# Kernel optimization log

Hardware: AMD Instinct MI355X
Metric: run time of the kernel (lower is better)

Reference implementation:

```python
import jax, jax.numpy as jnp
import numpy as np

NEG_SLOPE = 0.2  # both GATConv internal LeakyReLU and the module-level activation


def gat_conv(x, src, dst, W, a_src, a_dst, bias):
    """PyG GATConv (concat=True, add_self_loops handled by caller via src/dst).
    x: [N, Din]; W: [Din, H*C]; a_src, a_dst: [H, C]; bias: [H*C]."""
    N = x.shape[0]
    H, C = a_src.shape
    h = (x @ W).reshape(N, H, C)                       # [N, H, C]
    al_src = jnp.einsum('nhc,hc->nh', h, a_src)        # [N, H]
    al_dst = jnp.einsum('nhc,hc->nh', h, a_dst)        # [N, H]
    e = jax.nn.leaky_relu(al_src[src] + al_dst[dst], NEG_SLOPE)  # [E, H]
    # segment softmax over edges grouped by destination node
    m = jax.ops.segment_max(e, dst, num_segments=N)    # [N, H]
    ex = jnp.exp(e - m[dst])
    denom = jax.ops.segment_sum(ex, dst, num_segments=N)
    alpha = ex / denom[dst]                            # [E, H]
    out = jax.ops.segment_sum(alpha[:, :, None] * h[src], dst, num_segments=N)
    return out.reshape(N, H * C) + bias


def setup_inputs() -> dict:
    key = jax.random.key(0)
    N, E = 50000, 800000
    D_IN, HID, H = 128, 128, 2
    C = HID // H
    ks = jax.random.split(key, 20)
    inp = {
        'x': jax.random.normal(ks[0], (N, D_IN), dtype=jnp.float32),
        'edge_index': jax.random.randint(ks[1], (2, E), 0, N, dtype=jnp.int64),
    }
    dims = [D_IN, HID, HID]  # input dims of the 3 GATConv layers
    for i, din in enumerate(dims, start=1):
        s = 1.0 / np.sqrt(din)
        inp[f'W{i}'] = jax.random.normal(ks[2 + 4 * i], (din, HID), dtype=jnp.float32) * s
        inp[f'a_src{i}'] = jax.random.normal(ks[3 + 4 * i], (H, C), dtype=jnp.float32) * 0.1
        inp[f'a_dst{i}'] = jax.random.normal(ks[4 + 4 * i], (H, C), dtype=jnp.float32) * 0.1
        inp[f'b{i}'] = jnp.zeros((HID,), dtype=jnp.float32)
    inp['lin_w'] = jax.random.normal(ks[2], (HID, 1), dtype=jnp.float32) * (1.0 / np.sqrt(HID))
    inp['lin_b'] = jnp.zeros((1,), dtype=jnp.float32)
    return inp


def reference(x, edge_index, W1, a_src1, a_dst1, b1, W2, a_src2, a_dst2, b2,
              W3, a_src3, a_dst3, b3, lin_w, lin_b):
    N = x.shape[0]
    loops = jnp.arange(N, dtype=edge_index.dtype)
    src = jnp.concatenate([edge_index[0], loops])  # add_self_loops=True
    dst = jnp.concatenate([edge_index[1], loops])

    h = jax.nn.leaky_relu(gat_conv(x, src, dst, W1, a_src1, a_dst1, b1), NEG_SLOPE)
    # dropout is identity in eval mode (p=0.0)
    h = jax.nn.leaky_relu(h + gat_conv(h, src, dst, W2, a_src2, a_dst2, b2), NEG_SLOPE)
    h = jax.nn.leaky_relu(h + gat_conv(h, src, dst, W3, a_src3, a_dst3, b3), NEG_SLOPE)
    logits = (h @ lin_w + lin_b).squeeze(-1)  # [N]
    return logits
```

## Files before the change

kernel.cpp:

```cpp
#include <hip/hip_runtime.h>
#include <hip/hip_bf16.h>
#include <hip/hip_fp16.h>

#define LEAK 0.2f
#define BCAP 4096

typedef _Float16 half8  __attribute__((ext_vector_type(8)));
typedef _Float16 half4v __attribute__((ext_vector_type(4)));
typedef float    float4v __attribute__((ext_vector_type(4)));


__global__ __launch_bounds__(256) void k_binscatter(const int* __restrict__ esrc,
                                                    const int* __restrict__ edst,
                                                    int* __restrict__ gcnt,
                                                    unsigned int* __restrict__ binned,
                                                    int E, int ETOT, int NBK, int eb,
                                                    const float* __restrict__ W0,
                                                    const float* __restrict__ W1,
                                                    const float* __restrict__ W2,
                                                    _Float16* __restrict__ w16t) {
    int t = threadIdx.x;
    if (blockIdx.x >= eb) {
        __shared__ _Float16 tile[64][68];
        int bb = blockIdx.x - eb;
        int m = bb >> 2;
        int ti = (bb >> 1) & 1, tj = bb & 1;
        const float* src = (m == 0) ? W0 : (m == 1 ? W1 : W2);
        _Float16* dst = w16t + m * 16384;
        for (int idx = t; idx < 4096; idx += 256) {
            int r = idx >> 6, c = idx & 63;
            tile[r][c] = (_Float16)src[(ti * 64 + r) * 128 + tj * 64 + c];
        }
        __syncthreads();
        for (int idx = t; idx < 4096; idx += 256) {
            int c = idx >> 6, r = idx & 63;
            dst[(tj * 64 + c) * 128 + ti * 64 + r] = tile[r][c];
        }
        return;
    }
    __shared__ int lh[512];
    __shared__ int lbase[512];
    for (int b = t; b < NBK; b += 256) lh[b] = 0;
    __syncthreads();
    int base = blockIdx.x * 4096;
    unsigned int word[16]; int bb[16], rk[16];
    #pragma unroll
    for (int u = 0; u < 16; ++u) {
        int e = base + u * 256 + t;
        bb[u] = -1;
        if (e < ETOT) {
            int s, d;
            if (e < E) { s = esrc[e]; d = edst[e]; } else { s = d = e - E; }
            int b = d >> 7;
            bb[u] = b;
            rk[u] = atomicAdd(&lh[b], 1);
            word[u] = (unsigned int)s | ((unsigned int)(d & 127) << 17);
        }
    }
    __syncthreads();
    for (int b = t; b < NBK; b += 256) {
        int c = lh[b];
        lbase[b] = c ? atomicAdd(&gcnt[b], c) : 0;
    }
    __syncthreads();
    #pragma unroll
    for (int u = 0; u < 16; ++u)
        if (bb[u] >= 0)
            binned[(size_t)bb[u] * BCAP + lbase[bb[u]] + rk[u]] = word[u];
}

__global__ __launch_bounds__(256) void k_scatter2(const unsigned int* __restrict__ binned,
                                                  const int* __restrict__ gcnt,
                                                  int* __restrict__ off,
                                                  int* __restrict__ endv,
                                                  int* __restrict__ csr, int N) {
    __shared__ int deg[128];
    __shared__ int lcur[128];
    __shared__ int wt[2];
    int b = blockIdx.x, t = threadIdx.x;
    int n0 = b << 7;
    if (t < 128) deg[t] = 0;
    __syncthreads();
    int beg = b * BCAP, end = beg + gcnt[b];
    for (int i = beg + t; i < end; i += 256)
        atomicAdd(&deg[binned[i] >> 17], 1);
    __syncthreads();
    int v = 0, x = 0;
    if (t < 128) {
        v = deg[t];
        x = v;
        int lane = t & 63;
        #pragma unroll
        for (int o = 1; o < 64; o <<= 1) {
            int y = __shfl_up(x, o);
            if (lane >= o) x += y;
        }
        if (lane == 63) wt[t >> 6] = x;
    }
    __syncthreads();
    if (t < 128) {
        int excl = x - v + ((t >= 64) ? wt[0] : 0) + beg;
        lcur[t] = excl;
        int node = n0 + t;
        if (node < N) { off[node] = excl; endv[node] = excl + v; }
    }
    __syncthreads();
    for (int i = beg + t; i < end; i += 256) {
        unsigned int u = binned[i];
        int pos = atomicAdd(&lcur[u >> 17], 1);
        csr[pos] = (int)(u & 0x1FFFF);
    }
}


__global__ __launch_bounds__(256) void k_gemm_mfma(const void* __restrict__ Xv, int xfp16,
                                                   const _Float16* __restrict__ WhT,
                                                   const float* __restrict__ a_src,
                                                   const float* __restrict__ a_dst,
                                                   _Float16* __restrict__ Hout,
                                                   float* __restrict__ alsrc,
                                                   float* __restrict__ aldst, int N) {
    __shared__ _Float16 As[64][136];
    __shared__ float sS[64][2];
    __shared__ float sD[64][2];
    const int t = threadIdx.x;
    const int lane = t & 63, w = t >> 6;
    const int block_row = blockIdx.x * 64;

    if (t < 128) { sS[t >> 1][t & 1] = 0.f; sD[t >> 1][t & 1] = 0.f; }

    if (xfp16) {
        const _Float16* Xh = (const _Float16*)Xv;
        #pragma unroll
        for (int it = 0; it < 4; ++it) {
            int i = t + 256 * it;
            int row = i >> 4, c8 = i & 15;
            int gr = block_row + row;
            half8 hv = (half8){0,0,0,0,0,0,0,0};
            if (gr < N) hv = *(const half8*)(Xh + (size_t)gr * 128 + c8 * 8);
            *(half8*)(&As[row][c8 * 8]) = hv;
        }
    } else {
        const float* X = (const float*)Xv;
        #pragma unroll
        for (int it = 0; it < 8; ++it) {
            int i = t + 256 * it;
            int row = i >> 5, c4 = i & 31;
            int gr = block_row + row;
            float4 xv = make_float4(0.f, 0.f, 0.f, 0.f);
            if (gr < N) xv = *(const float4*)(X + (size_t)gr * 128 + c4 * 4);
            half4v hv;
            hv[0] = (_Float16)xv.x; hv[1] = (_Float16)xv.y;
            hv[2] = (_Float16)xv.z; hv[3] = (_Float16)xv.w;
            *(half4v*)(&As[row][c4 * 4]) = hv;
        }
    }

    const int l15 = lane & 15, kq = (lane >> 4) * 8;
    half8 bf[2][4];
    #pragma unroll
    for (int ntl = 0; ntl < 2; ++ntl) {
        int n0 = (w * 2 + ntl) * 16 + l15;
        #pragma unroll
        for (int kt = 0; kt < 4; ++kt)
            bf[ntl][kt] = *(const half8*)(WhT + (size_t)n0 * 128 + kt * 32 + kq);
    }
    __syncthreads();

    float4v acc[4][2];
    #pragma unroll
    for (int mt = 0; mt < 4; ++mt)
        #pragma unroll
        for (int ntl = 0; ntl < 2; ++ntl)
            acc[mt][ntl] = (float4v){0.f, 0.f, 0.f, 0.f};

    #pragma unroll
    for (int kt = 0; kt < 4; ++kt) {
        half8 a[4];
        #pragma unroll
        for (int mt = 0; mt < 4; ++mt)
            a[mt] = *(const half8*)(&As[mt * 16 + l15][kt * 32 + kq]);
        #pragma unroll
        for (int mt = 0; mt < 4; ++mt)
            #pragma unroll
            for (int ntl = 0; ntl < 2; ++ntl)
                acc[mt][ntl] = __builtin_amdgcn_mfma_f32_16x16x32_f16(
                    a[mt], bf[ntl][kt], acc[mt][ntl], 0, 0, 0);
    }

    #pragma unroll
    for (int mt = 0; mt < 4; ++mt) {
        int r0 = block_row + mt * 16 + (lane >> 4) * 4;
        #pragma unroll
        for (int ntl = 0; ntl < 2; ++ntl) {
            int col = (w * 2 + ntl) * 16 + l15;
            #pragma unroll
            for (int reg = 0; reg < 4; ++reg) {
                int r = r0 + reg;
                if (r < N) Hout[(size_t)r * 128 + col] = (_Float16)acc[mt][ntl][reg];
            }
        }
    }

    {
        int c0 = w * 32 + l15, c1 = c0 + 16;
        float as0 = a_src[c0], as1 = a_src[c1];
        float ad0 = a_dst[c0], ad1 = a_dst[c1];
        int head = w >> 1;
        #pragma unroll
        for (int mt = 0; mt < 4; ++mt) {
            #pragma unroll
            for (int reg = 0; reg < 4; ++reg) {
                float ps = (float)acc[mt][0][reg] * as0 + (float)acc[mt][1][reg] * as1;
                float pd = (float)acc[mt][0][reg] * ad0 + (float)acc[mt][1][reg] * ad1;
                #pragma unroll
                for (int o = 1; o < 16; o <<= 1) {
                    ps += __shfl_xor(ps, o);
                    pd += __shfl_xor(pd, o);
                }
                if (l15 == 0) {
                    int row = mt * 16 + (lane >> 4) * 4 + reg;
                    atomicAdd(&sS[row][head], ps);
                    atomicAdd(&sD[row][head], pd);
                }
            }
        }
    }
    __syncthreads();
    if (t < 128) {
        int row = t >> 1, head = t & 1;
        int gr = block_row + row;
        if (gr < N) {
            alsrc[gr * 2 + head] = sS[row][head];
            aldst[gr * 2 + head] = sD[row][head];
        }
    }
}


__global__ __launch_bounds__(256) void k_aggregate(
        const _Float16* __restrict__ H16,
        const float* __restrict__ alsrc,
        const float* __restrict__ aldst,
        const int* __restrict__ off, const int* __restrict__ endv,
        const int* __restrict__ csr,
        const float* __restrict__ bias,
        const _Float16* __restrict__ prev,
        _Float16* __restrict__ Out,
        const float* __restrict__ lw, const float* __restrict__ lb,
        float* __restrict__ logits, int N, int mode) {
    int wglobal = (int)((blockIdx.x * 256 + threadIdx.x) >> 6);
    int lane = threadIdx.x & 63;
    if (wglobal * 2 >= N) return;
    int half = lane >> 5;
    int hl = lane & 31;
    int node = wglobal * 2 + half;
    bool active = node < N;
    int nodeC = active ? node : (N - 1);
    int beg = off[nodeC];
    int end = active ? endv[nodeC] : beg;
    float ad0 = aldst[nodeC * 2], ad1 = aldst[nodeC * 2 + 1];

    int p = hl & 15;
    int q = hl >> 4;
    bool head0 = p < 8;
    const _Float16* hbase = H16 + p * 8;
    int hb = half << 5;

    float acc[8];
    #pragma unroll
    for (int k = 0; k < 8; ++k) acc[k] = 0.f;
    float dsum = 0.f;

    for (int base = beg; base < end; base += 32) {
        int i = base + hl;
        int s = 0; float w0 = 0.f, w1 = 0.f;
        if (i < end) {
            s = csr[i];
            float2 al = *(const float2*)(&alsrc[s * 2]);
            float e0 = al.x + ad0; e0 = e0 > 0.f ? e0 : LEAK * e0;
            float e1 = al.y + ad1; e1 = e1 > 0.f ? e1 : LEAK * e1;
            w0 = __expf(e0); w1 = __expf(e1);
        }
        int cnt = min(32, end - base);
        int iters = (cnt + 1) >> 1;
        int jj = 0;
        for (; jj + 4 <= iters; jj += 4) {
            int sl0 = hb + (jj << 1) + q;
            int sj0 = __shfl(s, sl0), sj1 = __shfl(s, sl0 + 2);
            int sj2 = __shfl(s, sl0 + 4), sj3 = __shfl(s, sl0 + 6);
            float w00 = __shfl(w0, sl0),     w10 = __shfl(w1, sl0);
            float w01 = __shfl(w0, sl0 + 2), w11 = __shfl(w1, sl0 + 2);
            float w02 = __shfl(w0, sl0 + 4), w12 = __shfl(w1, sl0 + 4);
            float w03 = __shfl(w0, sl0 + 6), w13 = __shfl(w1, sl0 + 6);
            float ws0 = head0 ? w00 : w10;
            float ws1 = head0 ? w01 : w11;
            float ws2 = head0 ? w02 : w12;
            float ws3 = head0 ? w03 : w13;
            uint4 r0 = *(const uint4*)(hbase + (size_t)sj0 * 128);
            uint4 r1 = *(const uint4*)(hbase + (size_t)sj1 * 128);
            uint4 r2 = *(const uint4*)(hbase + (size_t)sj2 * 128);
            uint4 r3 = *(const uint4*)(hbase + (size_t)sj3 * 128);
            const _Float16* h0 = (const _Float16*)&r0;
            const _Float16* h1 = (const _Float16*)&r1;
            const _Float16* h2 = (const _Float16*)&r2;
            const _Float16* h3 = (const _Float16*)&r3;
            #pragma unroll
            for (int k = 0; k < 8; ++k) acc[k] += ws0 * (float)h0[k];
            #pragma unroll
            for (int k = 0; k < 8; ++k) acc[k] += ws1 * (float)h1[k];
            #pragma unroll
            for (int k = 0; k < 8; ++k) acc[k] += ws2 * (float)h2[k];
            #pragma unroll
            for (int k = 0; k < 8; ++k) acc[k] += ws3 * (float)h3[k];
            dsum += (ws0 + ws1) + (ws2 + ws3);
        }
        for (; jj + 2 <= iters; jj += 2) {
            int sl0 = hb + (jj << 1) + q;
            int sj0 = __shfl(s, sl0), sj1 = __shfl(s, sl0 + 2);
            float w00 = __shfl(w0, sl0),     w10 = __shfl(w1, sl0);
            float w01 = __shfl(w0, sl0 + 2), w11 = __shfl(w1, sl0 + 2);
            float ws0 = head0 ? w00 : w10;
            float ws1 = head0 ? w01 : w11;
            uint4 r0 = *(const uint4*)(hbase + (size_t)sj0 * 128);
            uint4 r1 = *(const uint4*)(hbase + (size_t)sj1 * 128);
            const _Float16* h0 = (const _Float16*)&r0;
            const _Float16* h1 = (const _Float16*)&r1;
            #pragma unroll
            for (int k = 0; k < 8; ++k) acc[k] += ws0 * (float)h0[k];
            #pragma unroll
            for (int k = 0; k < 8; ++k) acc[k] += ws1 * (float)h1[k];
            dsum += ws0 + ws1;
        }
        if (jj < iters) {
            int sl = hb + (jj << 1) + q;
            int   sj = __shfl(s,  sl);
            float wa = __shfl(w0, sl);
            float wb = __shfl(w1, sl);
            float ws = head0 ? wa : wb;
            uint4 raw = *(const uint4*)(hbase + (size_t)sj * 128);
            const _Float16* h = (const _Float16*)&raw;
            #pragma unroll
            for (int k = 0; k < 8; ++k) acc[k] += ws * (float)h[k];
            dsum += ws;
        }
    }

    #pragma unroll
    for (int k = 0; k < 8; ++k) acc[k] += __shfl_xor(acc[k], 16);
    dsum += __shfl_xor(dsum, 16);

    if (q == 0 && active) {
        float inv = 1.f / dsum;
        int c0 = p * 8;
        float v[8];
        #pragma unroll
        for (int k = 0; k < 8; ++k) v[k] = acc[k] * inv + bias[c0 + k];
        if (mode >= 1) {
            half8 pv = *(const half8*)(prev + (size_t)node * 128 + c0);
            #pragma unroll
            for (int k = 0; k < 8; ++k) v[k] += (float)pv[k];
        }
        #pragma unroll
        for (int k = 0; k < 8; ++k) v[k] = v[k] > 0.f ? v[k] : LEAK * v[k];
        if (mode == 2) {
            float partial = 0.f;
            #pragma unroll
            for (int k = 0; k < 8; ++k) partial += v[k] * lw[c0 + k];
            partial += __shfl_xor(partial, 1);
            partial += __shfl_xor(partial, 2);
            partial += __shfl_xor(partial, 4);
            partial += __shfl_xor(partial, 8);
            if (hl == 0) logits[node] = partial + lb[0];
        } else {
            half8 ov;
            #pragma unroll
            for (int k = 0; k < 8; ++k) ov[k] = (_Float16)v[k];
            *(half8*)(Out + (size_t)node * 128 + c0) = ov;
        }
    }
}


extern "C" void kernel_launch(void* const* d_in, const int* in_sizes, int n_in,
                              void* d_out, int out_size, void* d_ws, size_t ws_size,
                              hipStream_t stream) {
    const float* x    = (const float*)d_in[0];
    const int*   edge = (const int*)d_in[1];
    const float* W[3]  = {(const float*)d_in[2], (const float*)d_in[6], (const float*)d_in[10]};
    const float* as[3] = {(const float*)d_in[3], (const float*)d_in[7], (const float*)d_in[11]};
    const float* ad[3] = {(const float*)d_in[4], (const float*)d_in[8], (const float*)d_in[12]};
    const float* bs[3] = {(const float*)d_in[5], (const float*)d_in[9], (const float*)d_in[13]};
    const float* lw = (const float*)d_in[14];
    const float* lb = (const float*)d_in[15];

    const int N    = in_sizes[0] / 128;
    const int E    = in_sizes[1] / 2;
    const int ETOT = E + N;
    const int NBK  = (N + 127) >> 7;

    char* base = (char*)d_ws;
    size_t o = 0;
    auto carve = [&](size_t bytes) {
        char* p = base + o;
        o = (o + bytes + 255) & ~(size_t)255;
        return p;
    };
    int*      off    = (int*)     carve((size_t)N * 4);
    int*      endv   = (int*)     carve((size_t)N * 4);
    int*      gcnt   = (int*)     carve((size_t)NBK * 4);
    unsigned* binned = (unsigned*)carve((size_t)NBK * BCAP * 4);
    int*      csr    = (int*)     carve((size_t)NBK * BCAP * 4);
    float*    alsrc  = (float*)   carve((size_t)N * 2 * 4);
    float*    aldst  = (float*)   carve((size_t)N * 2 * 4);
    _Float16* h16    = (_Float16*)carve((size_t)N * 128 * 2);
    _Float16* bufA   = (_Float16*)carve((size_t)N * 128 * 2);
    _Float16* bufB   = (_Float16*)carve((size_t)N * 128 * 2);
    _Float16* w16t   = (_Float16*)carve((size_t)3 * 16384 * 2);
    (void)ws_size; (void)n_in; (void)out_size;

    const int* esrc = edge;
    const int* edst = edge + E;

    int eb = (ETOT + 4095) / 4096;

    hipMemsetAsync(gcnt, 0, (size_t)NBK * 4, stream);

    k_binscatter<<<eb + 12, 256, 0, stream>>>(esrc, edst, gcnt, binned, E, ETOT, NBK, eb,
                                              W[0], W[1], W[2], w16t);
    k_scatter2<<<NBK, 256, 0, stream>>>(binned, gcnt, off, endv, csr, N);

    int gemm_blocks = (N + 63) / 64;
    int agg_blocks  = (N + 7) / 8;

    k_gemm_mfma<<<gemm_blocks, 256, 0, stream>>>(x, 0, w16t, as[0], ad[0], h16, alsrc, aldst, N);
    k_aggregate<<<agg_blocks, 256, 0, stream>>>(h16, alsrc, aldst, off, endv, csr,
                                                bs[0], nullptr, bufA, lw, lb, nullptr, N, 0);
    k_gemm_mfma<<<gemm_blocks, 256, 0, stream>>>(bufA, 1, w16t + 16384, as[1], ad[1], h16, alsrc, aldst, N);
    k_aggregate<<<agg_blocks, 256, 0, stream>>>(h16, alsrc, aldst, off, endv, csr,
                                                bs[1], bufA, bufB, lw, lb, nullptr, N, 1);
    k_gemm_mfma<<<gemm_blocks, 256, 0, stream>>>(bufB, 1, w16t + 32768, as[2], ad[2], h16, alsrc, aldst, N);
    k_aggregate<<<agg_blocks, 256, 0, stream>>>(h16, alsrc, aldst, off, endv, csr,
                                                bs[2], bufB, nullptr, lw, lb, (float*)d_out, N, 2);
}
```

Measured before the change: 276.1 us.

## Fuse CSR scatter into first GEMM launch, pack offsets, unroll gather by 8

After: 285.5 us. 3.4% more time.

```diff
diff --git a/kernel.cpp b/kernel.cpp
--- a/kernel.cpp
+++ b/kernel.cpp
@@ -69,15 +69,14 @@
             binned[(size_t)bb[u] * BCAP + lbase[bb[u]] + rk[u]] = word[u];
 }
 
-__global__ __launch_bounds__(256) void k_scatter2(const unsigned int* __restrict__ binned,
-                                                  const int* __restrict__ gcnt,
-                                                  int* __restrict__ off,
-                                                  int* __restrict__ endv,
-                                                  int* __restrict__ csr, int N) {
+__device__ void scatter2_body(int b, const unsigned int* __restrict__ binned,
+                              const int* __restrict__ gcnt,
+                              int2* __restrict__ offend,
+                              int* __restrict__ csr, int N) {
     __shared__ int deg[128];
     __shared__ int lcur[128];
     __shared__ int wt[2];
-    int b = blockIdx.x, t = threadIdx.x;
+    int t = threadIdx.x;
     int n0 = b << 7;
     if (t < 128) deg[t] = 0;
     __syncthreads();
@@ -102,7 +101,7 @@
         int excl = x - v + ((t >= 64) ? wt[0] : 0) + beg;
         lcur[t] = excl;
         int node = n0 + t;
-        if (node < N) { off[node] = excl; endv[node] = excl + v; }
+        if (node < N) offend[node] = make_int2(excl, excl + v);
     }
     __syncthreads();
     for (int i = beg + t; i < end; i += 256) {
@@ -119,7 +118,16 @@
                                                    const float* __restrict__ a_dst,
                                                    _Float16* __restrict__ Hout,
                                                    float* __restrict__ alsrc,
-                                                   float* __restrict__ aldst, int N) {
+                                                   float* __restrict__ aldst, int N,
+                                                   int gemm_nb,
+                                                   const unsigned int* __restrict__ binned,
+                                                   const int* __restrict__ gcnt,
+                                                   int2* __restrict__ offend,
+                                                   int* __restrict__ csr) {
+    if ((int)blockIdx.x >= gemm_nb) {
+        scatter2_body((int)blockIdx.x - gemm_nb, binned, gcnt, offend, csr, N);
+        return;
+    }
     __shared__ _Float16 As[64][136];
     __shared__ float sS[64][2];
     __shared__ float sD[64][2];
@@ -242,7 +250,7 @@
         const _Float16* __restrict__ H16,
         const float* __restrict__ alsrc,
         const float* __restrict__ aldst,
-        const int* __restrict__ off, const int* __restrict__ endv,
+        const int2* __restrict__ offend,
         const int* __restrict__ csr,
         const float* __restrict__ bias,
         const _Float16* __restrict__ prev,
@@ -257,9 +265,11 @@
     int node = wglobal * 2 + half;
     bool active = node < N;
     int nodeC = active ? node : (N - 1);
-    int beg = off[nodeC];
-    int end = active ? endv[nodeC] : beg;
-    float ad0 = aldst[nodeC * 2], ad1 = aldst[nodeC * 2 + 1];
+    int2 oe = offend[nodeC];
+    int beg = oe.x;
+    int end = active ? oe.y : beg;
+    float2 adv = *(const float2*)(aldst + (size_t)nodeC * 2);
+    float ad0 = adv.x, ad1 = adv.y;
 
     int p = hl & 15;
     int q = hl >> 4;
@@ -285,6 +295,28 @@
         int cnt = min(32, end - base);
         int iters = (cnt + 1) >> 1;
         int jj = 0;
+        for (; jj + 8 <= iters; jj += 8) {
+            int sl0 = hb + (jj << 1) + q;
+            int sjv[8]; float wsv[8];
+            #pragma unroll
+            for (int u = 0; u < 8; ++u) {
+                sjv[u] = __shfl(s, sl0 + 2 * u);
+                float wa = __shfl(w0, sl0 + 2 * u);
+                float wb = __shfl(w1, sl0 + 2 * u);
+                wsv[u] = head0 ? wa : wb;
+            }
+            uint4 rv[8];
+            #pragma unroll
+            for (int u = 0; u < 8; ++u)
+                rv[u] = *(const uint4*)(hbase + (size_t)sjv[u] * 128);
+            #pragma unroll
+            for (int u = 0; u < 8; ++u) {
+                const _Float16* h = (const _Float16*)&rv[u];
+                #pragma unroll
+                for (int k = 0; k < 8; ++k) acc[k] += wsv[u] * (float)h[k];
+                dsum += wsv[u];
+            }
+        }
         for (; jj + 4 <= iters; jj += 4) {
             int sl0 = hb + (jj << 1) + q;
             int sj0 = __shfl(s, sl0), sj1 = __shfl(s, sl0 + 2);
@@ -406,8 +438,7 @@
         o = (o + bytes + 255) & ~(size_t)255;
         return p;
     };
-    int*      off    = (int*)     carve((size_t)N * 4);
-    int*      endv   = (int*)     carve((size_t)N * 4);
+    int2*     offend = (int2*)    carve((size_t)N * 8);
     int*      gcnt   = (int*)     carve((size_t)NBK * 4);
     unsigned* binned = (unsigned*)carve((size_t)NBK * BCAP * 4);
     int*      csr    = (int*)     carve((size_t)NBK * BCAP * 4);
@@ -428,18 +459,23 @@
 
     k_binscatter<<<eb + 12, 256, 0, stream>>>(esrc, edst, gcnt, binned, E, ETOT, NBK, eb,
                                               W[0], W[1], W[2], w16t);
-    k_scatter2<<<NBK, 256, 0, stream>>>(binned, gcnt, off, endv, csr, N);
 
     int gemm_blocks = (N + 63) / 64;
     int agg_blocks  = (N + 7) / 8;
 
-    k_gemm_mfma<<<gemm_blocks, 256, 0, stream>>>(x, 0, w16t, as[0], ad[0], h16, alsrc, aldst, N);
-    k_aggregate<<<agg_blocks, 256, 0, stream>>>(h16, alsrc, aldst, off, endv, csr,
+    k_gemm_mfma<<<gemm_blocks + NBK, 256, 0, stream>>>(x, 0, w16t, as[0], ad[0], h16,
+                                                       alsrc, aldst, N, gemm_blocks,
+                                                       binned, gcnt, offend, csr);
+    k_aggregate<<<agg_blocks, 256, 0, stream>>>(h16, alsrc, aldst, offend, csr,
                                                 bs[0], nullptr, bufA, lw, lb, nullptr, N, 0);
-    k_gemm_mfma<<<gemm_blocks, 256, 0, stream>>>(bufA, 1, w16t + 16384, as[1], ad[1], h16, alsrc, aldst, N);
-    k_aggregate<<<agg_blocks, 256, 0, stream>>>(h16, alsrc, aldst, off, endv, csr,
+    k_gemm_mfma<<<gemm_blocks, 256, 0, stream>>>(bufA, 1, w16t + 16384, as[1], ad[1], h16,
+                                                 alsrc, aldst, N, gemm_blocks,
+                                                 binned, gcnt, offend, csr);
+    k_aggregate<<<agg_blocks, 256, 0, stream>>>(h16, alsrc, aldst, offend, csr,
                                                 bs[1], bufA, bufB, lw, lb, nullptr, N, 1);
-    k_gemm_mfma<<<gemm_blocks, 256, 0, stream>>>(bufB, 1, w16t + 32768, as[2], ad[2], h16, alsrc, aldst, N);
-    k_aggregate<<<agg_blocks, 256, 0, stream>>>(h16, alsrc, aldst, off, endv, csr,
+    k_gemm_mfma<<<gemm_blocks, 256, 0, stream>>>(bufB, 1, w16t + 32768, as[2], ad[2], h16,
+                                                 alsrc, aldst, N, gemm_blocks,
+                                                 binned, gcnt, offend, csr);
+    k_aggregate<<<agg_blocks, 256, 0, stream>>>(h16, alsrc, aldst, offend, csr,
                                                 bs[2], bufB, nullptr, lw, lb, (float*)d_out, N, 2);
 }
```
